# Kernel optimization log

Hardware: AMD Instinct MI355X
Metric: run time of the kernel (lower is better)

Reference implementation:

```python
import jax, jax.numpy as jnp
import numpy as np

M, K, N, E, TOPK = 4096, 2048, 5632, 8, 2


def setup_inputs() -> dict:
    key = jax.random.key(0)
    k1, k2, k3, k4, k5 = jax.random.split(key, 5)
    hidden_states = jax.random.normal(k1, (M, K), dtype=jnp.float32)
    # vLLM fused-MoE layout: w1 = [E, 2N, K] (gate+up), w2 = [E, K, N] (down)
    w1 = jax.random.normal(k2, (E, 2 * N, K), dtype=jnp.float32) * 0.02
    w2 = jax.random.normal(k3, (E, K, N), dtype=jnp.float32) * 0.02
    topk_ids = jax.random.randint(k4, (M, TOPK), 0, E, dtype=jnp.int32)
    raw = jax.random.uniform(k5, (M, TOPK), dtype=jnp.float32)
    topk_weights = raw / jnp.sum(raw, axis=-1, keepdims=True)  # router probs
    return {"hidden_states": hidden_states, "w1": w1, "w2": w2,
            "topk_weights": topk_weights, "topk_ids": topk_ids}


def reference(hidden_states, w1, w2, topk_weights, topk_ids):
    # gates[m, e] = sum over top-k slots routed to expert e of topk_weights
    onehot = jax.nn.one_hot(topk_ids, E, dtype=hidden_states.dtype)  # [M, topk, E]
    gates = jnp.einsum("mk,mke->me", topk_weights, onehot)           # [M, E]
    out = jnp.zeros_like(hidden_states)                              # [M, K]
    for e in range(E):  # fixed small expert count
        h = hidden_states @ w1[e].T            # [M, 2N] fused gate+up GEMM
        g, u = h[:, :N], h[:, N:]
        a = jax.nn.silu(g) * u                 # SiLU-GLU activation, [M, N]
        out = out + gates[:, e:e + 1] * (a @ w2[e].T)  # down GEMM + weighted combine
    return out
```

## Files before the change

kernel.cpp:

```cpp
#include <hip/hip_runtime.h>
#include <stdint.h>

#define GM 4096
#define GK 2048
#define GN 5632
#define GE 8
#define GTOPK 2

typedef __attribute__((ext_vector_type(4))) float f32x4;
typedef __attribute__((ext_vector_type(8))) short short8;
typedef __attribute__((ext_vector_type(4))) uint32_t u32x4;

__device__ __forceinline__ void gld16(const void* g, void* l) {
  __builtin_amdgcn_global_load_lds((const __attribute__((address_space(1))) void*)g,
                                   (__attribute__((address_space(3))) void*)l, 16, 0, 0);
}

__device__ __forceinline__ uint32_t pack2(float hi, float lo) {
  return __builtin_amdgcn_perm(__float_as_uint(hi), __float_as_uint(lo), 0x07060302u);
}

__device__ __forceinline__ unsigned short bf16rne(float f) {
  uint32_t u = __float_as_uint(f);
  u += 0x7FFFu + ((u >> 16) & 1u);
  return (unsigned short)(u >> 16);
}

__global__ void route_count(const int* __restrict__ ids, int* __restrict__ counts) {
  int i = blockIdx.x * blockDim.x + threadIdx.x;
  if (i < GM * GTOPK) atomicAdd(&counts[ids[i]], 1);
}

__global__ void route_scan(const int* __restrict__ counts, int* __restrict__ offs) {
  if (threadIdx.x == 0) {
    int s = 0;
    for (int e = 0; e < GE; ++e) { offs[e] = s; s += counts[e]; }
    offs[GE] = s;
  }
}

__global__ void route_scatter(const int* __restrict__ ids, const float* __restrict__ wts,
                              const int* __restrict__ offs, int* __restrict__ fill,
                              int* __restrict__ slot_token, float* __restrict__ slot_gate,
                              int* __restrict__ inv_slot) {
  int i = blockIdx.x * blockDim.x + threadIdx.x;
  if (i < GM * GTOPK) {
    int e = ids[i];
    int pos = offs[e] + atomicAdd(&fill[e], 1);
    slot_token[pos] = i / GTOPK;
    slot_gate[pos] = wts[i];
    inv_slot[i] = pos;
  }
}

__global__ void cvt_bf16(const float* __restrict__ x, unsigned short* __restrict__ y, int n8) {
  int i = blockIdx.x * blockDim.x + threadIdx.x;
  if (i >= n8) return;
  const f32x4* xp = (const f32x4*)x;
  f32x4 a = xp[2 * i], b = xp[2 * i + 1];
  u32x4 o;
  o.x = ((uint32_t)bf16rne(a.y) << 16) | bf16rne(a.x);
  o.y = ((uint32_t)bf16rne(a.w) << 16) | bf16rne(a.z);
  o.z = ((uint32_t)bf16rne(b.y) << 16) | bf16rne(b.x);
  o.w = ((uint32_t)bf16rne(b.w) << 16) | bf16rne(b.z);
  ((u32x4*)y)[i] = o;
}

template <int MODE>
__global__ __launch_bounds__(256, 2)
void moe_gemm_bf16(const unsigned short* __restrict__ A,
                   const unsigned short* __restrict__ Bw,
                   const int* __restrict__ offs,
                   const int* __restrict__ slot_token,
                   const float* __restrict__ slot_gate,
                   unsigned short* __restrict__ act,
                   float* __restrict__ scratch)
{
  constexpr int KR = (MODE == 1) ? GK : GN;
  const int e = blockIdx.z;
  const int segs = offs[e];
  const int segc = offs[e + 1] - segs;
  const int mtile = blockIdx.x;
  if (mtile * 128 >= segc) return;
  const int ntile = blockIdx.y;
  const int tid = threadIdx.x;
  const int w = tid >> 6, lane = tid & 63;
  const int wm = w >> 1, wn = w & 1;

  __shared__ __align__(16) char lds[32 * 1024];

  const unsigned short* Be = Bw + (size_t)e * (size_t)((MODE == 1) ? (2 * GN * GK) : (GK * GN));

  const unsigned short* asrc[4];
  const unsigned short* bsrc[4];
  {
    const int r16 = lane & 15;
    const int koff = (lane >> 4) * 8;
    #pragma unroll
    for (int c = 0; c < 4; ++c) {
      int u = c * 4 + w;
      int s = u >> 1, kk = u & 1;
      int slot = segs + mtile * 128 + s * 16 + r16;
      if (slot >= segs + segc) slot = segs;
      size_t arow = (MODE == 1) ? (size_t)slot_token[slot] : (size_t)slot;
      asrc[c] = A + arow * KR + (kk * 32 + koff);
      int brow;
      if (MODE == 1)
        brow = (s < 4) ? (ntile * 64 + s * 16 + r16) : (GN + ntile * 64 + (s - 4) * 16 + r16);
      else
        brow = ntile * 128 + s * 16 + r16;
      bsrc[c] = Be + (size_t)brow * KR + (kk * 32 + koff);
    }
  }
  char* adst[4];
  char* bdst[4];
  #pragma unroll
  for (int c = 0; c < 4; ++c) {
    adst[c] = lds + (c * 4 + w) * 1024;
    bdst[c] = lds + 16384 + (c * 4 + w) * 1024;
  }

  const f32x4 zero4 = {0.f, 0.f, 0.f, 0.f};
  f32x4 acc[4][4];
  #pragma unroll
  for (int a_ = 0; a_ < 4; ++a_)
    #pragma unroll
    for (int b_ = 0; b_ < 4; ++b_) acc[a_][b_] = zero4;

  const char* ldsA = lds + (wm * 4) * 2048 + lane * 16;

  for (int k0 = 0; k0 < KR; k0 += 64) {
    #pragma unroll
    for (int c = 0; c < 4; ++c) gld16(asrc[c] + k0, adst[c]);
    #pragma unroll
    for (int c = 0; c < 4; ++c) gld16(bsrc[c] + k0, bdst[c]);
    __syncthreads();

    #pragma unroll
    for (int kk = 0; kk < 2; ++kk) {
      short8 afr[4];
      #pragma unroll
      for (int mt = 0; mt < 4; ++mt)
        afr[mt] = *(const short8*)(ldsA + mt * 2048 + kk * 1024);
      #pragma unroll
      for (int j = 0; j < 4; ++j) {
        int sB = (MODE == 1) ? ((j < 2) ? (wn * 2 + j) : (4 + wn * 2 + (j - 2))) : (wn * 4 + j);
        short8 bfr = *(const short8*)(lds + 16384 + sB * 2048 + kk * 1024 + lane * 16);
        #pragma unroll
        for (int mt = 0; mt < 4; ++mt)
          acc[mt][j] = __builtin_amdgcn_mfma_f32_16x16x32_bf16(afr[mt], bfr, acc[mt][j], 0, 0, 0);
      }
    }
    __syncthreads();
  }

  int lcol = lane & 15;
  int rbase = (lane >> 4) * 4;
  if (MODE == 1) {
    #pragma unroll
    for (int mt = 0; mt < 4; ++mt) {
      int mloc = mtile * 128 + wm * 64 + mt * 16 + rbase;
      #pragma unroll
      for (int j = 0; j < 2; ++j) {
        int col = ntile * 64 + wn * 32 + j * 16 + lcol;
        f32x4 g = acc[mt][j], u = acc[mt][2 + j];
        #pragma unroll
        for (int r = 0; r < 4; ++r) {
          int ml = mloc + r;
          if (ml < segc) {
            float gv = g[r];
            float s = gv / (1.f + __expf(-gv));
            act[(size_t)(segs + ml) * GN + col] = bf16rne(s * u[r]);
          }
        }
      }
    }
  } else {
    #pragma unroll
    for (int mt = 0; mt < 4; ++mt) {
      int mloc = mtile * 128 + wm * 64 + mt * 16 + rbase;
      #pragma unroll
      for (int r = 0; r < 4; ++r) {
        int ml = mloc + r;
        if (ml < segc) {
          int slot = segs + ml;
          float gate = slot_gate[slot];
          float* srow = scratch + (size_t)slot * GK;
          #pragma unroll
          for (int j = 0; j < 4; ++j) {
            int col = ntile * 128 + wn * 64 + j * 16 + lcol;
            srow[col] = gate * acc[mt][j][r];
          }
        }
      }
    }
  }
}

__global__ void merge_out(const float* __restrict__ scratch, const int* __restrict__ inv,
                          float* __restrict__ out) {
  int i = blockIdx.x * blockDim.x + threadIdx.x;
  if (i >= GM * (GK / 8)) return;
  int token = i >> 8;
  int c = (i & 255) * 8;
  const float* s0 = scratch + (size_t)inv[2 * token] * GK + c;
  const float* s1 = scratch + (size_t)inv[2 * token + 1] * GK + c;
  f32x4 a0 = ((const f32x4*)s0)[0], a1 = ((const f32x4*)s0)[1];
  f32x4 b0 = ((const f32x4*)s1)[0], b1 = ((const f32x4*)s1)[1];
  float* o = out + (size_t)token * GK + c;
  ((f32x4*)o)[0] = a0 + b0;
  ((f32x4*)o)[1] = a1 + b1;
}

template <int MODE>
__global__ __launch_bounds__(256, 2)
void moe_gemm_f32(const unsigned short* __restrict__ A,
                  const float* __restrict__ B,
                  const int* __restrict__ offs,
                  const int* __restrict__ slot_token,
                  const float* __restrict__ slot_gate,
                  unsigned short* __restrict__ act,
                  float* __restrict__ out)
{
  constexpr int KR = (MODE == 1) ? GK : GN;
  const int e = blockIdx.z;
  const int segs = offs[e];
  const int segc = offs[e + 1] - segs;
  const int mtile = blockIdx.x;
  if (mtile * 128 >= segc) return;
  const int ntile = blockIdx.y;
  const int tid = threadIdx.x;
  const int w = tid >> 6, lane = tid & 63;
  const int wm = w >> 1, wn = w & 1;

  __shared__ __align__(16) char lds[24 * 1024];

  const float* Be = B + (size_t)e * (size_t)((MODE == 1) ? (2 * GN * GK) : (GK * GN));

  const char* aptr[2];
  {
    int m16 = lane & 15, h = lane >> 4;
    #pragma unroll
    for (int c = 0; c < 2; ++c) {
      int s = c * 4 + w;
      int slot = segs + mtile * 128 + s * 16 + m16;
      if (slot >= segs + segc) slot = segs;
      size_t arow = (MODE == 1) ? (size_t)slot_token[slot] : (size_t)slot;
      aptr[c] = (const char*)(A + arow * KR + h * 8);
    }
  }
  const char* bptr[4];
  {
    int n16 = lane & 15, k4hi = lane >> 4;
    #pragma unroll
    for (int c = 0; c < 4; ++c) {
      int q = c * 4 + w;
      int s = q >> 1, hh = q & 1;
      int k4 = hh * 4 + k4hi;
      int brow;
      if (MODE == 1)
        brow = (s < 4) ? (ntile * 64 + s * 16 + n16) : (GN + ntile * 64 + (s - 4) * 16 + n16);
      else
        brow = ntile * 128 + s * 16 + n16;
      bptr[c] = (const char*)(Be + (size_t)brow * KR + k4 * 4);
    }
  }
  char* ldsAdst0 = lds + w * 1024;
  char* ldsAdst1 = lds + (4 + w) * 1024;
  char* ldsBdst[4];
  #pragma unroll
  for (int c = 0; c < 4; ++c) ldsBdst[c] = lds + 8192 + (c * 4 + w) * 1024;

  const f32x4 zero4 = {0.f, 0.f, 0.f, 0.f};
  f32x4 acc[4][4];
  #pragma unroll
  for (int a_ = 0; a_ < 4; ++a_)
    #pragma unroll
    for (int b_ = 0; b_ < 4; ++b_) acc[a_][b_] = zero4;

  const char* ldsAfr = lds + (wm * 4) * 1024 + lane * 16;

  for (int k0 = 0; k0 < KR; k0 += 32) {
    gld16(aptr[0] + (size_t)k0 * 2, ldsAdst0);
    gld16(aptr[1] + (size_t)k0 * 2, ldsAdst1);
    #pragma unroll
    for (int c = 0; c < 4; ++c) gld16(bptr[c] + (size_t)k0 * 4, ldsBdst[c]);
    __syncthreads();

    short8 afr[4];
    #pragma unroll
    for (int mt = 0; mt < 4; ++mt) afr[mt] = *(const short8*)(ldsAfr + mt * 1024);
    #pragma unroll
    for (int j = 0; j < 4; ++j) {
      int sB = (MODE == 1) ? ((j < 2) ? (wn * 2 + j) : (4 + wn * 2 + j - 2)) : (wn * 4 + j);
      const char* lb = lds + 8192 + sB * 2048 + ((lane >> 4) * 32 + (lane & 15)) * 16;
      f32x4 b0 = *(const f32x4*)lb;
      f32x4 b1 = *(const f32x4*)(lb + 256);
      union { uint32_t u[4]; short8 s8; } bu;
      bu.u[0] = pack2(b0.y, b0.x);
      bu.u[1] = pack2(b0.w, b0.z);
      bu.u[2] = pack2(b1.y, b1.x);
      bu.u[3] = pack2(b1.w, b1.z);
      #pragma unroll
      for (int mt = 0; mt < 4; ++mt)
        acc[mt][j] = __builtin_amdgcn_mfma_f32_16x16x32_bf16(afr[mt], bu.s8, acc[mt][j], 0, 0, 0);
    }
    __syncthreads();
  }

  int lcol = lane & 15;
  int rbase = (lane >> 4) * 4;
  if (MODE == 1) {
    #pragma unroll
    for (int mt = 0; mt < 4; ++mt) {
      int mloc = mtile * 128 + wm * 64 + mt * 16 + rbase;
      #pragma unroll
      for (int j = 0; j < 2; ++j) {
        int col = ntile * 64 + wn * 32 + j * 16 + lcol;
        f32x4 g = acc[mt][j], u = acc[mt][2 + j];
        #pragma unroll
        for (int r = 0; r < 4; ++r) {
          int ml = mloc + r;
          if (ml < segc) {
            float gv = g[r];
            float s = gv / (1.f + __expf(-gv));
            act[(size_t)(segs + ml) * GN + col] = bf16rne(s * u[r]);
          }
        }
      }
    }
  } else {
    #pragma unroll
    for (int mt = 0; mt < 4; ++mt) {
      int mloc = mtile * 128 + wm * 64 + mt * 16 + rbase;
      #pragma unroll
      for (int r = 0; r < 4; ++r) {
        int ml = mloc + r;
        if (ml < segc) {
          int slot = segs + ml;
          float gate = slot_gate[slot];
          float* orow = out + (size_t)slot_token[slot] * GK;
          #pragma unroll
          for (int j = 0; j < 4; ++j) {
            int col = ntile * 128 + wn * 64 + j * 16 + lcol;
            atomicAdd(&orow[col], gate * acc[mt][j][r]);
          }
        }
      }
    }
  }
}

extern "C" void kernel_launch(void* const* d_in, const int* in_sizes, int n_in,
                              void* d_out, int out_size, void* d_ws, size_t ws_size,
                              hipStream_t stream) {
  const float* hs  = (const float*)d_in[0];
  const float* w1  = (const float*)d_in[1];
  const float* w2  = (const float*)d_in[2];
  const float* tkw = (const float*)d_in[3];
  const int*   tki = (const int*)d_in[4];
  float* out = (float*)d_out;

  char* ws = (char*)d_ws;
  int*   counts     = (int*)(ws + 0);
  int*   fill       = (int*)(ws + 64);
  int*   offs       = (int*)(ws + 128);
  int*   slot_token = (int*)(ws + 1024);
  float* slot_gate  = (float*)(ws + 1024 + 32768);
  int*   inv_slot   = (int*)(ws + 66560);
  unsigned short* hsb = (unsigned short*)(ws + 131072);
  unsigned short* act = (unsigned short*)(ws + 131072 + (size_t)GM * GK * 2);

  const size_t off_w1b = 131072 + (size_t)GM * GK * 2 + (size_t)GM * GTOPK * GN * 2;
  const size_t sz_w1b  = (size_t)GE * 2 * GN * GK * 2;
  const size_t off_w2b = off_w1b + sz_w1b;
  const size_t sz_w2b  = (size_t)GE * GK * GN * 2;
  const size_t off_scr = off_w2b + sz_w2b;
  const size_t sz_scr  = (size_t)GM * GTOPK * GK * 4;
  const size_t need    = off_scr + sz_scr;

  hipMemsetAsync(ws, 0, 1024, stream);

  route_count<<<(GM * GTOPK + 255) / 256, 256, 0, stream>>>(tki, counts);
  route_scan<<<1, 64, 0, stream>>>(counts, offs);
  route_scatter<<<(GM * GTOPK + 255) / 256, 256, 0, stream>>>(tki, tkw, offs, fill,
                                                              slot_token, slot_gate, inv_slot);
  cvt_bf16<<<(GM * GK / 8 + 255) / 256, 256, 0, stream>>>(hs, hsb, GM * GK / 8);

  if (ws_size >= need) {
    unsigned short* w1b = (unsigned short*)(ws + off_w1b);
    unsigned short* w2b = (unsigned short*)(ws + off_w2b);
    float* scratch = (float*)(ws + off_scr);
    const int n8w1 = GE * 2 * GN * GK / 8;
    const int n8w2 = GE * GK * GN / 8;
    cvt_bf16<<<(n8w1 + 255) / 256, 256, 0, stream>>>(w1, w1b, n8w1);
    cvt_bf16<<<(n8w2 + 255) / 256, 256, 0, stream>>>(w2, w2b, n8w2);

    moe_gemm_bf16<1><<<dim3(64, GN / 64, GE), 256, 0, stream>>>(hsb, w1b, offs, slot_token,
                                                                slot_gate, act, nullptr);
    moe_gemm_bf16<2><<<dim3(64, GK / 128, GE), 256, 0, stream>>>(act, w2b, offs, slot_token,
                                                                 slot_gate, nullptr, scratch);
    merge_out<<<(GM * (GK / 8) + 255) / 256, 256, 0, stream>>>(scratch, inv_slot, out);
  } else {
    hipMemsetAsync(d_out, 0, (size_t)out_size * sizeof(float), stream);
    moe_gemm_f32<1><<<dim3(64, GN / 64, GE), 256, 0, stream>>>(hsb, w1, offs, slot_token,
                                                               slot_gate, act, nullptr);
    moe_gemm_f32<2><<<dim3(64, GK / 128, GE), 256, 0, stream>>>(act, w2, offs, slot_token,
                                                                slot_gate, nullptr, out);
  }
}
```

Measured before the change: 5.056 ms.

## Double-buffer LDS tiles to overlap global loads with MFMA compute

Doubles the shared-memory tile buffer and restructures the K loop so the next 64-wide K slice is loaded into the alternate buffer while MFMAs consume the current one. This cuts one barrier per iteration and is meant to hide global-to-LDS load latency behind compute. In exchange, LDS use per block doubles to 64 KB, which can lower the number of resident blocks per CU.

```diff
diff --git a/kernel.cpp b/kernel.cpp
--- a/kernel.cpp
+++ b/kernel.cpp
@@ -87,7 +87,7 @@
   const int w = tid >> 6, lane = tid & 63;
   const int wm = w >> 1, wn = w & 1;
 
-  __shared__ __align__(16) char lds[32 * 1024];
+  __shared__ __align__(16) char lds[2][32 * 1024];
 
   const unsigned short* Be = Bw + (size_t)e * (size_t)((MODE == 1) ? (2 * GN * GK) : (GK * GN));
 
@@ -112,13 +112,6 @@
       bsrc[c] = Be + (size_t)brow * KR + (kk * 32 + koff);
     }
   }
-  char* adst[4];
-  char* bdst[4];
-  #pragma unroll
-  for (int c = 0; c < 4; ++c) {
-    adst[c] = lds + (c * 4 + w) * 1024;
-    bdst[c] = lds + 16384 + (c * 4 + w) * 1024;
-  }
 
   const f32x4 zero4 = {0.f, 0.f, 0.f, 0.f};
   f32x4 acc[4][4];
@@ -127,15 +120,30 @@
     #pragma unroll
     for (int b_ = 0; b_ < 4; ++b_) acc[a_][b_] = zero4;
 
-  const char* ldsA = lds + (wm * 4) * 2048 + lane * 16;
-
-  for (int k0 = 0; k0 < KR; k0 += 64) {
-    #pragma unroll
-    for (int c = 0; c < 4; ++c) gld16(asrc[c] + k0, adst[c]);
-    #pragma unroll
-    for (int c = 0; c < 4; ++c) gld16(bsrc[c] + k0, bdst[c]);
-    __syncthreads();
-
+  constexpr int NT = KR / 64;
+
+  {
+    char* base = lds[0];
+    #pragma unroll
+    for (int c = 0; c < 4; ++c) gld16(asrc[c], base + (c * 4 + w) * 1024);
+    #pragma unroll
+    for (int c = 0; c < 4; ++c) gld16(bsrc[c], base + 16384 + (c * 4 + w) * 1024);
+  }
+  __syncthreads();
+
+  int cur = 0;
+  for (int t = 0; t < NT; ++t) {
+    if (t + 1 < NT) {
+      char* nb = lds[cur ^ 1];
+      const int k0 = (t + 1) * 64;
+      #pragma unroll
+      for (int c = 0; c < 4; ++c) gld16(asrc[c] + k0, nb + (c * 4 + w) * 1024);
+      #pragma unroll
+      for (int c = 0; c < 4; ++c) gld16(bsrc[c] + k0, nb + 16384 + (c * 4 + w) * 1024);
+    }
+
+    const char* base = lds[cur];
+    const char* ldsA = base + (wm * 4) * 2048 + lane * 16;
     #pragma unroll
     for (int kk = 0; kk < 2; ++kk) {
       short8 afr[4];
@@ -145,13 +153,14 @@
       #pragma unroll
       for (int j = 0; j < 4; ++j) {
         int sB = (MODE == 1) ? ((j < 2) ? (wn * 2 + j) : (4 + wn * 2 + (j - 2))) : (wn * 4 + j);
-        short8 bfr = *(const short8*)(lds + 16384 + sB * 2048 + kk * 1024 + lane * 16);
+        short8 bfr = *(const short8*)(base + 16384 + sB * 2048 + kk * 1024 + lane * 16);
         #pragma unroll
         for (int mt = 0; mt < 4; ++mt)
           acc[mt][j] = __builtin_amdgcn_mfma_f32_16x16x32_bf16(afr[mt], bfr, acc[mt][j], 0, 0, 0);
       }
     }
     __syncthreads();
+    cur ^= 1;
   }
 
   int lcol = lane & 15;
```

Result: no change. 5.150 ms (+1.9%).
